# Kernel tuning notes

Hardware: AMD Instinct MI355X
Metric: run time of the kernel (lower is better)

## Reference

```python
import jax, jax.numpy as jnp
import numpy as np

N = 2048      # nodes
E = 65536     # edges (avg degree 32)
IN_C = 512
OUT_C = 512
KP1 = 3       # K=2 Chebyshev -> 3 terms


def setup_inputs() -> dict:
    key = jax.random.key(0)
    k0, k1, k2, k3, k4 = jax.random.split(key, 5)
    X_real = jax.random.normal(k0, (N, IN_C), jnp.float32)
    X_imag = jax.random.normal(k1, (N, IN_C), jnp.float32)
    edges = jax.random.randint(k2, (2, E), 0, N).astype(jnp.int64)
    edge_weight = jax.random.uniform(k3, (E,), jnp.float32)
    q = jnp.float32(0.25)
    stdv = 1.0 / np.sqrt(OUT_C)
    weight = jax.random.uniform(k4, (KP1, IN_C, OUT_C), jnp.float32, -stdv, stdv)
    bias = jnp.zeros((1, OUT_C), jnp.float32)
    return {"X_real": X_real, "X_imag": X_imag, "edges": edges, "q": q,
            "edge_weight": edge_weight, "weight": weight, "bias": bias}


def _cheb_laplacians(edges, edge_weight, q):
    """QinDirect_hermitian_decomp_sparse (norm=True, laplacian=True, max_eigen=2,
    gcn_appr=False) followed by cheb_poly_sparse with K=2. Returns stacked
    real/imag parts of [T0, T1, T2], each [KP1, N, N]."""
    f, e = edges[0], edges[1]
    A = jnp.zeros((N, N), jnp.float32).at[f, e].add(edge_weight)
    A_sym = 0.5 * (A + A.T)
    deg = A_sym.sum(axis=0)
    dinv = jnp.where(deg == 0.0, 1.0, deg) ** -0.5
    A_norm = dinv[:, None] * A_sym * dinv[None, :]   # D^-1/2 A_sym D^-1/2
    theta = (2.0 * jnp.pi) * q * (A - A.T)           # phase matrix
    # L = I - exp(i*theta) .* A_norm ; scaled (2/max_eigen)*L - I with max_eigen=2
    # => L_scaled = -exp(i*theta) .* A_norm
    L1_re = -jnp.cos(theta) * A_norm
    L1_im = -jnp.sin(theta) * A_norm
    eye = jnp.eye(N, dtype=jnp.float32)
    # T2 = 2*L1@L1 - I (complex square in real arithmetic)
    L2_re = 2.0 * (L1_re @ L1_re - L1_im @ L1_im) - eye
    L2_im = 2.0 * (L1_re @ L1_im + L1_im @ L1_re)
    L_re = jnp.stack([eye, L1_re, L2_re])                        # [KP1,N,N]
    L_im = jnp.stack([jnp.zeros((N, N), jnp.float32), L1_im, L2_im])
    return L_re, L_im


def reference(X_real, X_imag, edges, q, edge_weight, weight, bias):
    L_re, L_im = _cheb_laplacians(edges, edge_weight, q)
    # NOTE: original forward swaps the lists: L_norm_real = L_img, L_norm_imag = L_real.
    mr, mi = L_im, L_re
    # per term k: real_k = (mr_k@Xr - mi_k@Xi) @ W_k ; imag_k = (mi_k@Xr + mr_k@Xi) @ W_k
    Ar = jnp.einsum('knm,mf->knf', mr, X_real) - jnp.einsum('knm,mf->knf', mi, X_imag)
    Ai = jnp.einsum('knm,mf->knf', mi, X_real) + jnp.einsum('knm,mf->knf', mr, X_imag)
    real = jnp.einsum('knf,kfo->no', Ar, weight)   # sum over K terms
    imag = jnp.einsum('knf,kfo->no', Ai, weight)
    return real + bias, imag + bias
```

## Files before the change

kernel.cpp:

```cpp
#include <hip/hip_runtime.h>
#include <hip/hip_bf16.h>
#include <math.h>

#define NN 2048
#define CC 512
#define NEDGE 65536

typedef __hip_bfloat16 bf16;
typedef __attribute__((ext_vector_type(8))) short short8;
typedef __attribute__((ext_vector_type(4))) float floatx4;
typedef __attribute__((ext_vector_type(2))) float floatx2;
typedef __attribute__((ext_vector_type(4))) unsigned short us4;
typedef __attribute__((ext_vector_type(2))) unsigned short us2;

static constexpr float TWO_PI_F = 6.2831853071795864769f;

__device__ __forceinline__ unsigned short f2bu(float f) {
    bf16 h = __float2bfloat16(f);
    return *reinterpret_cast<unsigned short*>(&h);
}
__device__ __forceinline__ float bu2f(unsigned short u) {
    return __uint_as_float(((unsigned)u) << 16);
}

__device__ __forceinline__ void gld16(const void* g, void* l) {
    __builtin_amdgcn_global_load_lds(
        (const __attribute__((address_space(1))) unsigned int*)(unsigned long long)(uintptr_t)g,
        (__attribute__((address_space(3))) unsigned int*)(unsigned long long)(uintptr_t)l,
        16, 0, 0);
}

__global__ void detect_k(const unsigned int* __restrict__ qword,
                         const unsigned int* __restrict__ ewords,
                         int* __restrict__ flag) {
    int lane = threadIdx.x;
    unsigned int w0 = ewords[2 * lane + 1];
    unsigned int w1 = ewords[128 + 2 * lane + 1];
    unsigned long long b = __ballot((w0 | w1) != 0u);
    if (lane == 0) {
        flag[0] = ((qword[0] & 0xFFFFu) == 0x3E80u) ? 1 : 0;
        flag[1] = (b == 0ull) ? 1 : 0;
    }
}


__global__ void scatter_edges_k(const void* __restrict__ edges,
                                const void* __restrict__ w,
                                float* __restrict__ A, float* __restrict__ AT,
                                const int* __restrict__ flag) {
    int e = blockIdx.x * 256 + threadIdx.x;
    if (e >= NEDGE) return;
    int f, t;
    if (flag[1]) {
        f = (int)((const long long*)edges)[e];
        t = (int)((const long long*)edges)[NEDGE + e];
    } else {
        f = ((const int*)edges)[e];
        t = ((const int*)edges)[NEDGE + e];
    }
    float wv = flag[0] ? __bfloat162float(((const bf16*)w)[e]) : ((const float*)w)[e];
    f &= (NN - 1); t &= (NN - 1);
    atomicAdd(&A[(size_t)f * NN + t], wv);
    atomicAdd(&AT[(size_t)t * NN + f], wv);
}

__global__ __launch_bounds__(256) void dinv_compact_k(
    const float* __restrict__ A, const float* __restrict__ AT,
    float* __restrict__ dinv, int* __restrict__ ecol,
    floatx2* __restrict__ em, int* __restrict__ ecnt)
{
    int i = blockIdx.x, t = threadIdx.x;
    __shared__ int s_cnt;
    __shared__ int   c_col[256];
    __shared__ float c_s[256], c_d[256];
    __shared__ float red[256];
    if (t == 0) s_cnt = 0;
    __syncthreads();
    const floatx4* A4 = (const floatx4*)(A + (size_t)i * NN);
    const floatx4* B4 = (const floatx4*)(AT + (size_t)i * NN);
    float sum = 0.f;
#pragma unroll
    for (int it = 0; it < 2; ++it) {
        int g = it * 256 + t;
        floatx4 a = A4[g], b = B4[g];
#pragma unroll
        for (int l = 0; l < 4; ++l) {
            float av = a[l], bv = b[l];
            float s = av + bv;
            sum += s;
            if (s != 0.f) {
                int slot = atomicAdd(&s_cnt, 1);
                if (slot < 256) { c_col[slot] = g * 4 + l; c_s[slot] = s; c_d[slot] = av - bv; }
            }
        }
    }
    red[t] = sum;
    __syncthreads();
    for (int off = 128; off > 0; off >>= 1) {
        if (t < off) red[t] += red[t + off];
        __syncthreads();
    }
    if (t == 0) {
        float d = 0.5f * red[0];
        if (d == 0.f) d = 1.f;
        dinv[i] = rsqrtf(d);
    }
    int n = s_cnt; if (n > 256) n = 256;
    if (t == 0) ecnt[i] = n;
    if (t < n) {
        ecol[i * 256 + t] = c_col[t];
        em[i * 256 + t]   = (floatx2){c_s[t], c_d[t]};
    }
}

__global__ __launch_bounds__(256) void mval_k(
    const float* __restrict__ dinv, const void* __restrict__ qp,
    const int* __restrict__ ecol, floatx2* __restrict__ em,
    const int* __restrict__ ecnt, const int* __restrict__ flag)
{
    int i = blockIdx.x, t = threadIdx.x;
    if (t >= ecnt[i]) return;
    float qv = flag[0] ? __bfloat162float(((const bf16*)qp)[0]) : ((const float*)qp)[0];
    int j = ecol[i * 256 + t];
    floatx2 sd = em[i * 256 + t];
    float an = dinv[i] * (0.5f * sd.x) * dinv[j];
    float th = TWO_PI_F * qv * sd.y;
    float sn, cs;
    sincosf(th, &sn, &cs);
    em[i * 256 + t] = (floatx2){-cs * an, sn * an};
}

__global__ __launch_bounds__(1024) void pack_inputs_k(
    const void* __restrict__ xr, const void* __restrict__ xi,
    const void* __restrict__ Wt,
    bf16* __restrict__ Af, bf16* __restrict__ WT, void* __restrict__ Xc,
    const int* __restrict__ flag) {
    __shared__ float t1[32][33];
    int tid = threadIdx.x;
    int tx = tid & 31, ty = tid >> 5;
    int bx = blockIdx.x;
    int isbf = flag[0];
    if (bx < 1024) {
        int c0 = (bx & 15) * 32, r0 = (bx >> 4) * 32;
        size_t sidx = (size_t)(r0 + ty) * CC + c0 + tx;
        float fr, fi;
        if (isbf) {
            fr = __bfloat162float(((const bf16*)xr)[sidx]);
            fi = __bfloat162float(((const bf16*)xi)[sidx]);
        } else {
            fr = ((const float*)xr)[sidx];
            fi = ((const float*)xi)[sidx];
        }
        int r = r0 + ty, c = c0 + tx;
        Af[(size_t)r * 1536 + c]        = __float2bfloat16(-fi);
        Af[(size_t)(NN + r) * 1536 + c] = __float2bfloat16(fr);
        float fro = __shfl_xor(fr, 1);
        float fio = __shfl_xor(fi, 1);
        if ((tx & 1) == 0) {
            int g = c >> 1;
            if (isbf) {
                *(us4*)((bf16*)Xc + (size_t)r * 1024 + 4 * g) =
                    (us4){f2bu(fr), f2bu(fro), f2bu(fi), f2bu(fio)};
            } else {
                ((floatx4*)Xc)[(size_t)r * 256 + g] = (floatx4){fr, fro, fi, fio};
            }
        }
    } else {
        int bw = bx - 1024;
        int k0 = (bw % 48) * 32, o0 = (bw / 48) * 32;
        size_t sidx = (size_t)(k0 + ty) * CC + o0 + tx;
        t1[ty][tx] = isbf ? __bfloat162float(((const bf16*)Wt)[sidx])
                          : ((const float*)Wt)[sidx];
        __syncthreads();
        WT[(size_t)(o0 + ty) * 1536 + k0 + tx] = __float2bfloat16(t1[tx][ty]);
    }
}

template<int EPI>
__global__ __launch_bounds__(256) void spmm_k(
    const int* __restrict__ ecol, const floatx2* __restrict__ em,
    const int* __restrict__ ecnt,
    const void* __restrict__ xr, const void* __restrict__ xi,
    const void* __restrict__ Xc, const bf16* __restrict__ Z1in,
    bf16* __restrict__ Z1out, bf16* __restrict__ Af,
    const int* __restrict__ flag)
{
    int i = blockIdx.x, t = threadIdx.x;
    int isbf = flag[0];
    int n = ecnt[i];
    __shared__ int   sc[256];
    __shared__ float sre[256], sim[256];
    if (t < n) {
        sc[t] = ecol[i * 256 + t];
        floatx2 m = em[i * 256 + t];
        sre[t] = m.x; sim[t] = m.y;
    }
    __syncthreads();
    float ar0 = 0.f, ar1 = 0.f, ai0 = 0.f, ai1 = 0.f;

    if (EPI == 1 && !isbf) {
        const floatx4* X4 = (const floatx4*)Xc;
#pragma unroll 4
        for (int s = 0; s < n; ++s) {
            int j = sc[s];
            float re = sre[s], im = sim[s];
            floatx4 v = X4[(((unsigned)j) << 8) + t];
            ar0 += re * v.x - im * v.z;  ai0 += re * v.z + im * v.x;
            ar1 += re * v.y - im * v.w;  ai1 += re * v.w + im * v.y;
        }
    } else {
        const us4* X4 = (const us4*)(EPI == 1 ? Xc : (const void*)Z1in);
#pragma unroll 4
        for (int s = 0; s < n; ++s) {
            int j = sc[s];
            float re = sre[s], im = sim[s];
            us4 v = X4[(((unsigned)j) << 8) + t];
            float vr0 = bu2f(v.x), vr1 = bu2f(v.y);
            float vi0 = bu2f(v.z), vi1 = bu2f(v.w);
            ar0 += re * vr0 - im * vi0;  ai0 += re * vi0 + im * vr0;
            ar1 += re * vr1 - im * vi1;  ai1 += re * vi1 + im * vr1;
        }
    }

    if (EPI == 1) {
        *(us4*)(Z1out + (size_t)i * 1024 + 4 * t) =
            (us4){f2bu(ar0), f2bu(ar1), f2bu(ai0), f2bu(ai1)};
        *(us2*)(Af + (size_t)i * 1536 + 512 + 2 * t)        = (us2){f2bu(-ai0), f2bu(-ai1)};
        *(us2*)(Af + (size_t)(NN + i) * 1536 + 512 + 2 * t) = (us2){f2bu(ar0), f2bu(ar1)};
    } else {
        float xr0, xr1, xi0, xi1;
        if (isbf) {
            us2 vr = *(const us2*)((const bf16*)xr + (size_t)i * CC + 2 * t);
            us2 vi = *(const us2*)((const bf16*)xi + (size_t)i * CC + 2 * t);
            xr0 = bu2f(vr.x); xr1 = bu2f(vr.y);
            xi0 = bu2f(vi.x); xi1 = bu2f(vi.y);
        } else {
            floatx2 vr = *(const floatx2*)((const float*)xr + (size_t)i * CC + 2 * t);
            floatx2 vi = *(const floatx2*)((const float*)xi + (size_t)i * CC + 2 * t);
            xr0 = vr.x; xr1 = vr.y; xi0 = vi.x; xi1 = vi.y;
        }
        float vre0 = 2.f * ar0 - xr0, vre1 = 2.f * ar1 - xr1;
        float vim0 = 2.f * ai0 - xi0, vim1 = 2.f * ai1 - xi1;
        *(us2*)(Af + (size_t)(NN + i) * 1536 + 1024 + 2 * t) = (us2){f2bu(vre0), f2bu(vre1)};
        *(us2*)(Af + (size_t)i * 1536 + 1024 + 2 * t)        = (us2){f2bu(-vim0), f2bu(-vim1)};
    }
}

__global__ void epi3_k(const bf16* __restrict__ Pb, const void* __restrict__ bias,
                       void* __restrict__ out, const int* __restrict__ flag) {
    int idx = blockIdx.x * 256 + threadIdx.x;
    if (idx >= 4096 * CC) return;
    int c = idx & (CC - 1);
    float s = 0.f;
#pragma unroll
    for (int z = 0; z < 4; ++z)
        s += __bfloat162float(Pb[(size_t)z * 4096 * CC + idx]);
    float bb = flag[0] ? __bfloat162float(((const bf16*)bias)[c]) : ((const float*)bias)[c];
    float o = s + bb;
    if (flag[0]) ((bf16*)out)[idx] = __float2bfloat16(o);
    else         ((float*)out)[idx] = o;
}

__global__ __launch_bounds__(256) void gemm_sk_k(
    const bf16* __restrict__ Ab, const bf16* __restrict__ BTb,
    int M, int N, int K, int klen,
    bf16* __restrict__ Pb)
{
    __shared__ bf16 sA[128 * 64];
    __shared__ bf16 sB[128 * 64];
    int tid = threadIdx.x;
    int w = tid >> 6, lane = tid & 63;
    int row0 = blockIdx.y * 128, col0 = blockIdx.x * 128;
    int kbase = blockIdx.z * klen;
    int wave_m = (w >> 1) * 64, wave_n = (w & 1) * 64;
    int lm = lane & 15, lq = lane >> 4;

    int srow = lane >> 3;
    int sg   = lane & 7;
    int scol = (sg ^ srow) * 8;
    const bf16 *gA[4], *gB[4];
    bf16 *lA[4], *lB[4];
#pragma unroll
    for (int i = 0; i < 4; ++i) {
        int c = w * 4 + i;
        int row = c * 8 + srow;
        gA[i] = Ab  + (size_t)(row0 + row) * K + kbase + scol;
        gB[i] = BTb + (size_t)(col0 + row) * K + kbase + scol;
        lA[i] = sA + c * 512 + lane * 8;
        lB[i] = sB + c * 512 + lane * 8;
    }

    floatx4 acc[4][4];
#pragma unroll
    for (int mf = 0; mf < 4; ++mf)
#pragma unroll
        for (int nf = 0; nf < 4; ++nf)
            acc[mf][nf] = (floatx4){0.f, 0.f, 0.f, 0.f};

    for (int kk = 0; kk < klen; kk += 64) {
        __syncthreads();
#pragma unroll
        for (int i = 0; i < 4; ++i) {
            gld16(gA[i] + kk, lA[i]);
            gld16(gB[i] + kk, lB[i]);
        }
        __syncthreads();
#pragma unroll
        for (int ks = 0; ks < 2; ++ks) {
            short8 af[4], bfv[4];
#pragma unroll
            for (int mf = 0; mf < 4; ++mf) {
                int row = wave_m + mf * 16 + lm;
                int g = (ks * 4 + lq) ^ (row & 7);
                af[mf] = *(const short8*)&sA[row * 64 + g * 8];
            }
#pragma unroll
            for (int nf = 0; nf < 4; ++nf) {
                int row = wave_n + nf * 16 + lm;
                int g = (ks * 4 + lq) ^ (row & 7);
                bfv[nf] = *(const short8*)&sB[row * 64 + g * 8];
            }
#pragma unroll
            for (int mf = 0; mf < 4; ++mf)
#pragma unroll
                for (int nf = 0; nf < 4; ++nf)
                    acc[mf][nf] = __builtin_amdgcn_mfma_f32_16x16x32_bf16(
                        af[mf], bfv[nf], acc[mf][nf], 0, 0, 0);
        }
    }

    bf16* slice = Pb + (size_t)blockIdx.z * M * N;
#pragma unroll
    for (int mf = 0; mf < 4; ++mf) {
#pragma unroll
        for (int nf = 0; nf < 4; ++nf) {
            int gcol = col0 + wave_n + nf * 16 + lm;
#pragma unroll
            for (int r = 0; r < 4; ++r) {
                int grow = row0 + wave_m + mf * 16 + lq * 4 + r;
                slice[(size_t)grow * N + gcol] = __float2bfloat16(acc[mf][nf][r]);
            }
        }
    }
}


extern "C" void kernel_launch(void* const* d_in, const int* in_sizes, int n_in,
                              void* d_out, int out_size, void* d_ws, size_t ws_size,
                              hipStream_t stream) {
    const void* Xr_in = d_in[0];
    const void* Xi_in = d_in[1];
    const void* edges = d_in[2];
    const void* q     = d_in[3];
    const void* ew    = d_in[4];
    const void* Wt    = d_in[5];
    const void* bias  = d_in[6];

    char* base = (char*)d_ws;
    const size_t MB = 1024 * 1024;
    float*   A    = (float*)(base);
    float*   AT   = (float*)(base + 16 * MB);
    void*    Xc   = (void*)(base);
    bf16*    Af   = (bf16*)(base + 32 * MB);
    bf16*    WT   = (bf16*)(base + 44 * MB);
    bf16*    Z1c  = (bf16*)(base + 46 * MB);
    float*   dinv = (float*)(base + 50 * MB);
    int*     flag = (int*)  (base + 50 * MB + 16 * 1024);
    int*     ecnt = (int*)  (base + 50 * MB + 32 * 1024);
    bf16*    Pb   = (bf16*)(base + 56 * MB);
    int*     ecol = (int*)  (base + 56 * MB);
    floatx2* em   = (floatx2*)(base + 58 * MB);

    detect_k<<<1, 64, 0, stream>>>((const unsigned int*)q, (const unsigned int*)edges, flag);
    hipMemsetAsync(A, 0, 32 * MB, stream);

    scatter_edges_k<<<NEDGE / 256, 256, 0, stream>>>(edges, ew, A, AT, flag);
    dinv_compact_k<<<NN, 256, 0, stream>>>(A, AT, dinv, ecol, em, ecnt);
    mval_k<<<NN, 256, 0, stream>>>(dinv, q, ecol, em, ecnt, flag);
    pack_inputs_k<<<1792, 1024, 0, stream>>>(Xr_in, Xi_in, Wt, Af, WT, Xc, flag);

    spmm_k<1><<<NN, 256, 0, stream>>>(ecol, em, ecnt, Xr_in, Xi_in, Xc,
                                      nullptr, Z1c, Af, flag);
    spmm_k<2><<<NN, 256, 0, stream>>>(ecol, em, ecnt, Xr_in, Xi_in, nullptr,
                                      Z1c, nullptr, Af, flag);

    gemm_sk_k<<<dim3(CC / 128, 4096 / 128, 4), 256, 0, stream>>>(
        Af, WT, 4096, CC, 1536, 384, Pb);
    epi3_k<<<(4096 * CC) / 256, 256, 0, stream>>>(Pb, bias, d_out, flag);
}
```

Before: 178.9 us.

## Fuse graph build, packing and both SpMM passes into one persistent kernel

Replaces the detect, scatter, degree/compaction, mval, pack and two SpMM launches with a single persistent kernel of 512 blocks that uses atomic-counter grid barriers between phases. Each block keeps its four rows' compacted edge lists in shared memory, so the ecol/em round trips through global memory go away, and it zeroes A/AT itself instead of relying on a memset. This removes launch overhead and global traffic between stages. In exchange it depends on all 512 blocks being co-resident for the spin barriers, and it lowers per-phase parallelism (4 rows per block, 256-thread blocks for packing).

```diff
diff --git a/kernel.cpp b/kernel.cpp
--- a/kernel.cpp
+++ b/kernel.cpp
@@ -5,6 +5,8 @@
 #define NN 2048
 #define CC 512
 #define NEDGE 65536
+#define MGRID 512
+#define MROWS 4
 
 typedef __hip_bfloat16 bf16;
 typedef __attribute__((ext_vector_type(8))) short short8;
@@ -30,210 +32,213 @@
         16, 0, 0);
 }
 
-__global__ void detect_k(const unsigned int* __restrict__ qword,
-                         const unsigned int* __restrict__ ewords,
-                         int* __restrict__ flag) {
-    int lane = threadIdx.x;
-    unsigned int w0 = ewords[2 * lane + 1];
-    unsigned int w1 = ewords[128 + 2 * lane + 1];
-    unsigned long long b = __ballot((w0 | w1) != 0u);
-    if (lane == 0) {
-        flag[0] = ((qword[0] & 0xFFFFu) == 0x3E80u) ? 1 : 0;
-        flag[1] = (b == 0ull) ? 1 : 0;
-    }
-}
-
-
-__global__ void scatter_edges_k(const void* __restrict__ edges,
-                                const void* __restrict__ w,
-                                float* __restrict__ A, float* __restrict__ AT,
-                                const int* __restrict__ flag) {
-    int e = blockIdx.x * 256 + threadIdx.x;
-    if (e >= NEDGE) return;
-    int f, t;
-    if (flag[1]) {
-        f = (int)((const long long*)edges)[e];
-        t = (int)((const long long*)edges)[NEDGE + e];
-    } else {
-        f = ((const int*)edges)[e];
-        t = ((const int*)edges)[NEDGE + e];
-    }
-    float wv = flag[0] ? __bfloat162float(((const bf16*)w)[e]) : ((const float*)w)[e];
-    f &= (NN - 1); t &= (NN - 1);
-    atomicAdd(&A[(size_t)f * NN + t], wv);
-    atomicAdd(&AT[(size_t)t * NN + f], wv);
-}
-
-__global__ __launch_bounds__(256) void dinv_compact_k(
-    const float* __restrict__ A, const float* __restrict__ AT,
-    float* __restrict__ dinv, int* __restrict__ ecol,
-    floatx2* __restrict__ em, int* __restrict__ ecnt)
+__device__ __forceinline__ void gbar(int* ctr, int k) {
+    __syncthreads();
+    __threadfence();
+    if (threadIdx.x == 0) {
+        atomicAdd(&ctr[k], 1);
+        while (atomicAdd(&ctr[k], 0) < (int)gridDim.x) __builtin_amdgcn_s_sleep(8);
+    }
+    __syncthreads();
+    __threadfence();
+}
+
+__global__ __launch_bounds__(256, 4) void mega_k(
+    const void* __restrict__ xr, const void* __restrict__ xi,
+    const void* __restrict__ edges, const void* __restrict__ qp,
+    const void* __restrict__ ew, const void* __restrict__ Wt,
+    float* __restrict__ A, float* __restrict__ AT,
+    bf16* __restrict__ Af, bf16* __restrict__ WTo,
+    void* __restrict__ Xc, bf16* __restrict__ Z1c,
+    float* __restrict__ dinv, int* __restrict__ flagw, int* __restrict__ ctr)
 {
-    int i = blockIdx.x, t = threadIdx.x;
-    __shared__ int s_cnt;
-    __shared__ int   c_col[256];
-    __shared__ float c_s[256], c_d[256];
+    __shared__ float t1[32][33];
     __shared__ float red[256];
-    if (t == 0) s_cnt = 0;
+    __shared__ short e_col[MROWS][256];
+    __shared__ float e_v1[MROWS][256], e_v2[MROWS][256];
+    __shared__ int   e_n[MROWS];
+    __shared__ int   s_cnt;
+
+    int bid = blockIdx.x, t = threadIdx.x;
+    int isbf = ((((const unsigned*)qp)[0] & 0xFFFFu) == 0x3E80u);
+
+    {
+        floatx4 z = (floatx4){0.f, 0.f, 0.f, 0.f};
+        floatx4* Z4 = (floatx4*)A;
+#pragma unroll
+        for (int k = 0; k < 16; ++k)
+            Z4[((size_t)(k * MGRID + bid)) * 256 + t] = z;
+    }
+    for (int r = bid; r < NN; r += MGRID) {
+        float fr0, fr1, fi0, fi1;
+        if (isbf) {
+            us2 vr = *(const us2*)((const bf16*)xr + (size_t)r * CC + 2 * t);
+            us2 vi = *(const us2*)((const bf16*)xi + (size_t)r * CC + 2 * t);
+            fr0 = bu2f(vr.x); fr1 = bu2f(vr.y); fi0 = bu2f(vi.x); fi1 = bu2f(vi.y);
+        } else {
+            floatx2 vr = *(const floatx2*)((const float*)xr + (size_t)r * CC + 2 * t);
+            floatx2 vi = *(const floatx2*)((const float*)xi + (size_t)r * CC + 2 * t);
+            fr0 = vr.x; fr1 = vr.y; fi0 = vi.x; fi1 = vi.y;
+        }
+        *(us2*)(Af + (size_t)r * 1536 + 2 * t)        = (us2){f2bu(-fi0), f2bu(-fi1)};
+        *(us2*)(Af + (size_t)(NN + r) * 1536 + 2 * t) = (us2){f2bu(fr0), f2bu(fr1)};
+        if (isbf)
+            ((us4*)Xc)[(size_t)r * 256 + t] = (us4){f2bu(fr0), f2bu(fr1), f2bu(fi0), f2bu(fi1)};
+        else
+            ((floatx4*)Xc)[(size_t)r * 256 + t] = (floatx4){fr0, fr1, fi0, fi1};
+    }
+    for (int bw = bid; bw < 768; bw += MGRID) {
+        int k0 = (bw % 48) * 32, o0 = (bw / 48) * 32;
+        int tx = t & 31, ty = t >> 5;
+        __syncthreads();
+#pragma unroll
+        for (int rr = 0; rr < 32; rr += 8) {
+            size_t sidx = (size_t)(k0 + ty + rr) * CC + o0 + tx;
+            t1[ty + rr][tx] = isbf ? __bfloat162float(((const bf16*)Wt)[sidx])
+                                   : ((const float*)Wt)[sidx];
+        }
+        __syncthreads();
+#pragma unroll
+        for (int rr = 0; rr < 32; rr += 8)
+            WTo[(size_t)(o0 + ty + rr) * 1536 + k0 + tx] = __float2bfloat16(t1[tx][ty + rr]);
+    }
+    if (bid == 0 && t < 64) {
+        unsigned w0 = ((const unsigned*)edges)[2 * t + 1];
+        unsigned w1 = ((const unsigned*)edges)[128 + 2 * t + 1];
+        unsigned long long b = __ballot((w0 | w1) != 0u);
+        if (t == 0) { flagw[0] = isbf; flagw[1] = (b == 0ull) ? 1 : 0; }
+    }
+    gbar(ctr, 0);
+
+    {
+        int i64 = flagw[1];
+        int e = bid * 256 + t;
+        if (e < NEDGE) {
+            int f, to;
+            if (i64) {
+                f  = (int)((const long long*)edges)[e];
+                to = (int)((const long long*)edges)[NEDGE + e];
+            } else {
+                f  = ((const int*)edges)[e];
+                to = ((const int*)edges)[NEDGE + e];
+            }
+            float wv = isbf ? __bfloat162float(((const bf16*)ew)[e]) : ((const float*)ew)[e];
+            f &= (NN - 1); to &= (NN - 1);
+            atomicAdd(&A [(size_t)f * NN + to], wv);
+            atomicAdd(&AT[(size_t)to * NN + f], wv);
+        }
+    }
+    gbar(ctr, 1);
+
+    for (int ii = 0; ii < MROWS; ++ii) {
+        int i = bid + ii * MGRID;
+        __syncthreads();
+        if (t == 0) s_cnt = 0;
+        __syncthreads();
+        const floatx4* A4 = (const floatx4*)(A + (size_t)i * NN);
+        const floatx4* B4 = (const floatx4*)(AT + (size_t)i * NN);
+        float sum = 0.f;
+#pragma unroll
+        for (int it = 0; it < 2; ++it) {
+            int g = it * 256 + t;
+            floatx4 a = A4[g], b = B4[g];
+#pragma unroll
+            for (int l = 0; l < 4; ++l) {
+                float av = a[l], bv = b[l], s = av + bv;
+                sum += s;
+                if (s != 0.f) {
+                    int slot = atomicAdd(&s_cnt, 1);
+                    if (slot < 256) {
+                        e_col[ii][slot] = (short)(g * 4 + l);
+                        e_v1[ii][slot] = s;
+                        e_v2[ii][slot] = av - bv;
+                    }
+                }
+            }
+        }
+        red[t] = sum;
+        __syncthreads();
+        for (int off = 128; off > 0; off >>= 1) {
+            if (t < off) red[t] += red[t + off];
+            __syncthreads();
+        }
+        if (t == 0) {
+            float d = 0.5f * red[0];
+            if (d == 0.f) d = 1.f;
+            dinv[i] = rsqrtf(d);
+            e_n[ii] = (s_cnt > 256) ? 256 : s_cnt;
+        }
+    }
+    gbar(ctr, 2);
+
+    float qv = isbf ? __bfloat162float(((const bf16*)qp)[0]) : ((const float*)qp)[0];
+    for (int ii = 0; ii < MROWS; ++ii) {
+        int i = bid + ii * MGRID;
+        int n = e_n[ii];
+        if (t < n) {
+            int j = (int)e_col[ii][t];
+            float an = dinv[i] * (0.5f * e_v1[ii][t]) * dinv[j];
+            float th = TWO_PI_F * qv * e_v2[ii][t];
+            float sn, cs;
+            sincosf(th, &sn, &cs);
+            e_v1[ii][t] = -cs * an;
+            e_v2[ii][t] =  sn * an;
+        }
+    }
     __syncthreads();
-    const floatx4* A4 = (const floatx4*)(A + (size_t)i * NN);
-    const floatx4* B4 = (const floatx4*)(AT + (size_t)i * NN);
-    float sum = 0.f;
-#pragma unroll
-    for (int it = 0; it < 2; ++it) {
-        int g = it * 256 + t;
-        floatx4 a = A4[g], b = B4[g];
-#pragma unroll
-        for (int l = 0; l < 4; ++l) {
-            float av = a[l], bv = b[l];
-            float s = av + bv;
-            sum += s;
-            if (s != 0.f) {
-                int slot = atomicAdd(&s_cnt, 1);
-                if (slot < 256) { c_col[slot] = g * 4 + l; c_s[slot] = s; c_d[slot] = av - bv; }
-            }
-        }
-    }
-    red[t] = sum;
-    __syncthreads();
-    for (int off = 128; off > 0; off >>= 1) {
-        if (t < off) red[t] += red[t + off];
-        __syncthreads();
-    }
-    if (t == 0) {
-        float d = 0.5f * red[0];
-        if (d == 0.f) d = 1.f;
-        dinv[i] = rsqrtf(d);
-    }
-    int n = s_cnt; if (n > 256) n = 256;
-    if (t == 0) ecnt[i] = n;
-    if (t < n) {
-        ecol[i * 256 + t] = c_col[t];
-        em[i * 256 + t]   = (floatx2){c_s[t], c_d[t]};
-    }
-}
-
-__global__ __launch_bounds__(256) void mval_k(
-    const float* __restrict__ dinv, const void* __restrict__ qp,
-    const int* __restrict__ ecol, floatx2* __restrict__ em,
-    const int* __restrict__ ecnt, const int* __restrict__ flag)
-{
-    int i = blockIdx.x, t = threadIdx.x;
-    if (t >= ecnt[i]) return;
-    float qv = flag[0] ? __bfloat162float(((const bf16*)qp)[0]) : ((const float*)qp)[0];
-    int j = ecol[i * 256 + t];
-    floatx2 sd = em[i * 256 + t];
-    float an = dinv[i] * (0.5f * sd.x) * dinv[j];
-    float th = TWO_PI_F * qv * sd.y;
-    float sn, cs;
-    sincosf(th, &sn, &cs);
-    em[i * 256 + t] = (floatx2){-cs * an, sn * an};
-}
-
-__global__ __launch_bounds__(1024) void pack_inputs_k(
-    const void* __restrict__ xr, const void* __restrict__ xi,
-    const void* __restrict__ Wt,
-    bf16* __restrict__ Af, bf16* __restrict__ WT, void* __restrict__ Xc,
-    const int* __restrict__ flag) {
-    __shared__ float t1[32][33];
-    int tid = threadIdx.x;
-    int tx = tid & 31, ty = tid >> 5;
-    int bx = blockIdx.x;
-    int isbf = flag[0];
-    if (bx < 1024) {
-        int c0 = (bx & 15) * 32, r0 = (bx >> 4) * 32;
-        size_t sidx = (size_t)(r0 + ty) * CC + c0 + tx;
-        float fr, fi;
-        if (isbf) {
-            fr = __bfloat162float(((const bf16*)xr)[sidx]);
-            fi = __bfloat162float(((const bf16*)xi)[sidx]);
+    for (int ii = 0; ii < MROWS; ++ii) {
+        int i = bid + ii * MGRID;
+        int n = e_n[ii];
+        float ar0 = 0.f, ar1 = 0.f, ai0 = 0.f, ai1 = 0.f;
+        if (!isbf) {
+            const floatx4* X4 = (const floatx4*)Xc;
+#pragma unroll 4
+            for (int s = 0; s < n; ++s) {
+                int j = (int)e_col[ii][s];
+                float re = e_v1[ii][s], im = e_v2[ii][s];
+                floatx4 v = X4[(((unsigned)j) << 8) + t];
+                ar0 += re * v.x - im * v.z;  ai0 += re * v.z + im * v.x;
+                ar1 += re * v.y - im * v.w;  ai1 += re * v.w + im * v.y;
+            }
         } else {
-            fr = ((const float*)xr)[sidx];
-            fi = ((const float*)xi)[sidx];
-        }
-        int r = r0 + ty, c = c0 + tx;
-        Af[(size_t)r * 1536 + c]        = __float2bfloat16(-fi);
-        Af[(size_t)(NN + r) * 1536 + c] = __float2bfloat16(fr);
-        float fro = __shfl_xor(fr, 1);
-        float fio = __shfl_xor(fi, 1);
-        if ((tx & 1) == 0) {
-            int g = c >> 1;
-            if (isbf) {
-                *(us4*)((bf16*)Xc + (size_t)r * 1024 + 4 * g) =
-                    (us4){f2bu(fr), f2bu(fro), f2bu(fi), f2bu(fio)};
-            } else {
-                ((floatx4*)Xc)[(size_t)r * 256 + g] = (floatx4){fr, fro, fi, fio};
-            }
-        }
-    } else {
-        int bw = bx - 1024;
-        int k0 = (bw % 48) * 32, o0 = (bw / 48) * 32;
-        size_t sidx = (size_t)(k0 + ty) * CC + o0 + tx;
-        t1[ty][tx] = isbf ? __bfloat162float(((const bf16*)Wt)[sidx])
-                          : ((const float*)Wt)[sidx];
-        __syncthreads();
-        WT[(size_t)(o0 + ty) * 1536 + k0 + tx] = __float2bfloat16(t1[tx][ty]);
-    }
-}
-
-template<int EPI>
-__global__ __launch_bounds__(256) void spmm_k(
-    const int* __restrict__ ecol, const floatx2* __restrict__ em,
-    const int* __restrict__ ecnt,
-    const void* __restrict__ xr, const void* __restrict__ xi,
-    const void* __restrict__ Xc, const bf16* __restrict__ Z1in,
-    bf16* __restrict__ Z1out, bf16* __restrict__ Af,
-    const int* __restrict__ flag)
-{
-    int i = blockIdx.x, t = threadIdx.x;
-    int isbf = flag[0];
-    int n = ecnt[i];
-    __shared__ int   sc[256];
-    __shared__ float sre[256], sim[256];
-    if (t < n) {
-        sc[t] = ecol[i * 256 + t];
-        floatx2 m = em[i * 256 + t];
-        sre[t] = m.x; sim[t] = m.y;
-    }
-    __syncthreads();
-    float ar0 = 0.f, ar1 = 0.f, ai0 = 0.f, ai1 = 0.f;
-
-    if (EPI == 1 && !isbf) {
-        const floatx4* X4 = (const floatx4*)Xc;
+            const us4* X4 = (const us4*)Xc;
+#pragma unroll 4
+            for (int s = 0; s < n; ++s) {
+                int j = (int)e_col[ii][s];
+                float re = e_v1[ii][s], im = e_v2[ii][s];
+                us4 v = X4[(((unsigned)j) << 8) + t];
+                float vr0 = bu2f(v.x), vr1 = bu2f(v.y);
+                float vi0 = bu2f(v.z), vi1 = bu2f(v.w);
+                ar0 += re * vr0 - im * vi0;  ai0 += re * vi0 + im * vr0;
+                ar1 += re * vr1 - im * vi1;  ai1 += re * vi1 + im * vr1;
+            }
+        }
+        *(us4*)(Z1c + (size_t)i * 1024 + 4 * t) = (us4){f2bu(ar0), f2bu(ar1), f2bu(ai0), f2bu(ai1)};
+        *(us2*)(Af + (size_t)i * 1536 + 512 + 2 * t)        = (us2){f2bu(-ai0), f2bu(-ai1)};
+        *(us2*)(Af + (size_t)(NN + i) * 1536 + 512 + 2 * t) = (us2){f2bu(ar0), f2bu(ar1)};
+    }
+    gbar(ctr, 3);
+
+    for (int ii = 0; ii < MROWS; ++ii) {
+        int i = bid + ii * MGRID;
+        int n = e_n[ii];
+        float ar0 = 0.f, ar1 = 0.f, ai0 = 0.f, ai1 = 0.f;
+        const us4* X4 = (const us4*)Z1c;
 #pragma unroll 4
         for (int s = 0; s < n; ++s) {
-            int j = sc[s];
-            float re = sre[s], im = sim[s];
-            floatx4 v = X4[(((unsigned)j) << 8) + t];
-            ar0 += re * v.x - im * v.z;  ai0 += re * v.z + im * v.x;
-            ar1 += re * v.y - im * v.w;  ai1 += re * v.w + im * v.y;
-        }
-    } else {
-        const us4* X4 = (const us4*)(EPI == 1 ? Xc : (const void*)Z1in);
-#pragma unroll 4
-        for (int s = 0; s < n; ++s) {
-            int j = sc[s];
-            float re = sre[s], im = sim[s];
+            int j = (int)e_col[ii][s];
+            float re = e_v1[ii][s], im = e_v2[ii][s];
             us4 v = X4[(((unsigned)j) << 8) + t];
             float vr0 = bu2f(v.x), vr1 = bu2f(v.y);
             float vi0 = bu2f(v.z), vi1 = bu2f(v.w);
             ar0 += re * vr0 - im * vi0;  ai0 += re * vi0 + im * vr0;
             ar1 += re * vr1 - im * vi1;  ai1 += re * vi1 + im * vr1;
         }
-    }
-
-    if (EPI == 1) {
-        *(us4*)(Z1out + (size_t)i * 1024 + 4 * t) =
-            (us4){f2bu(ar0), f2bu(ar1), f2bu(ai0), f2bu(ai1)};
-        *(us2*)(Af + (size_t)i * 1536 + 512 + 2 * t)        = (us2){f2bu(-ai0), f2bu(-ai1)};
-        *(us2*)(Af + (size_t)(NN + i) * 1536 + 512 + 2 * t) = (us2){f2bu(ar0), f2bu(ar1)};
-    } else {
         float xr0, xr1, xi0, xi1;
         if (isbf) {
             us2 vr = *(const us2*)((const bf16*)xr + (size_t)i * CC + 2 * t);
             us2 vi = *(const us2*)((const bf16*)xi + (size_t)i * CC + 2 * t);
-            xr0 = bu2f(vr.x); xr1 = bu2f(vr.y);
-            xi0 = bu2f(vi.x); xi1 = bu2f(vi.y);
+            xr0 = bu2f(vr.x); xr1 = bu2f(vr.y); xi0 = bu2f(vi.x); xi1 = bu2f(vi.y);
         } else {
             floatx2 vr = *(const floatx2*)((const float*)xr + (size_t)i * CC + 2 * t);
             floatx2 vi = *(const floatx2*)((const float*)xi + (size_t)i * CC + 2 * t);
@@ -358,31 +363,21 @@
 
     char* base = (char*)d_ws;
     const size_t MB = 1024 * 1024;
-    float*   A    = (float*)(base);
-    float*   AT   = (float*)(base + 16 * MB);
-    void*    Xc   = (void*)(base);
-    bf16*    Af   = (bf16*)(base + 32 * MB);
-    bf16*    WT   = (bf16*)(base + 44 * MB);
-    bf16*    Z1c  = (bf16*)(base + 46 * MB);
-    float*   dinv = (float*)(base + 50 * MB);
-    int*     flag = (int*)  (base + 50 * MB + 16 * 1024);
-    int*     ecnt = (int*)  (base + 50 * MB + 32 * 1024);
-    bf16*    Pb   = (bf16*)(base + 56 * MB);
-    int*     ecol = (int*)  (base + 56 * MB);
-    floatx2* em   = (floatx2*)(base + 58 * MB);
-
-    detect_k<<<1, 64, 0, stream>>>((const unsigned int*)q, (const unsigned int*)edges, flag);
-    hipMemsetAsync(A, 0, 32 * MB, stream);
-
-    scatter_edges_k<<<NEDGE / 256, 256, 0, stream>>>(edges, ew, A, AT, flag);
-    dinv_compact_k<<<NN, 256, 0, stream>>>(A, AT, dinv, ecol, em, ecnt);
-    mval_k<<<NN, 256, 0, stream>>>(dinv, q, ecol, em, ecnt, flag);
-    pack_inputs_k<<<1792, 1024, 0, stream>>>(Xr_in, Xi_in, Wt, Af, WT, Xc, flag);
-
-    spmm_k<1><<<NN, 256, 0, stream>>>(ecol, em, ecnt, Xr_in, Xi_in, Xc,
-                                      nullptr, Z1c, Af, flag);
-    spmm_k<2><<<NN, 256, 0, stream>>>(ecol, em, ecnt, Xr_in, Xi_in, nullptr,
-                                      Z1c, nullptr, Af, flag);
+    float* A    = (float*)(base);
+    float* AT   = (float*)(base + 16 * MB);
+    bf16*  Af   = (bf16*)(base + 32 * MB);
+    bf16*  WT   = (bf16*)(base + 44 * MB);
+    void*  Xc   = (void*)(base + 46 * MB);
+    float* dinv = (float*)(base + 54 * MB);
+    int*   flag = (int*)  (base + 54 * MB + 16 * 1024);
+    int*   ctr  = (int*)  (base + 54 * MB + 64 * 1024);
+    bf16*  Z1c  = (bf16*)(base + 55 * MB);
+    bf16*  Pb   = (bf16*)(base + 56 * MB);
+
+    hipMemsetAsync(ctr, 0, 256, stream);
+
+    mega_k<<<MGRID, 256, 0, stream>>>(Xr_in, Xi_in, edges, q, ew, Wt,
+                                      A, AT, Af, WT, Xc, Z1c, dinv, flag, ctr);
 
     gemm_sk_k<<<dim3(CC / 128, 4096 / 128, 4), 256, 0, stream>>>(
         Af, WT, 4096, CC, 1536, 384, Pb);
```

New measurement: 575.6 us. 222% more time.
